# Optimization experiments

Hardware: AMD Instinct MI355X
Metric: run time of the kernel (lower is better)

## Reference

```python
import jax, jax.numpy as jnp
import numpy as np


def _iir_forward(b_coeff, rho, psi, u_in, y_init, u_init):
    # Coefficient computation: stable 2nd-order resonator parameterization
    r = jax.nn.sigmoid(rho)
    theta = jnp.pi * jax.nn.sigmoid(psi)
    a1 = -2.0 * r * jnp.cos(theta)
    a2 = r * r

    B, T = u_in.shape
    nb = b_coeff.shape[0]  # number of FIR taps (n_b)

    # FIR (moving-average) part, fully vectorized over batch and time:
    # v[t] = sum_k b[k] * u[t-k]; past inputs come from u_init = [u[-1], u[-2], ...]
    u_ext = jnp.concatenate([u_init[:, ::-1], u_in], axis=1)  # [B, T + nb - 1], time-ordered
    v = jnp.zeros_like(u_in)
    for k in range(nb):  # small fixed loop over filter taps
        v = v + b_coeff[k] * jax.lax.dynamic_slice_in_dim(u_ext, nb - 1 - k, T, axis=1)

    # AR (recursive) part: y[t] = v[t] - a1*y[t-1] - a2*y[t-2]  (sequential scan over time)
    def step(carry, v_t):
        y1, y2 = carry  # y[t-1], y[t-2], each [B]
        y = v_t - a1 * y1 - a2 * y2
        return (y, y1), y

    init = (y_init[:, 0], y_init[:, 1])  # [y[-1], y[-2]] per lfiltic convention
    _, y = jax.lax.scan(step, init, v.T)  # y: [T, B]
    return y.T  # [B, T]


def setup_inputs() -> dict:
    key = jax.random.key(0)
    k1, k2, k3, k4 = jax.random.split(key, 4)
    B, T, NB = 1024, 16384, 3
    return {
        "b_coeff": 0.1 * jax.random.normal(k1, (NB,), dtype=jnp.float32),
        "rho": jnp.asarray(jax.random.normal(k2, (), dtype=jnp.float32) + 0.9),
        "psi": jnp.asarray(jax.random.normal(k3, (), dtype=jnp.float32) * 0.5),
        "u_in": jax.random.normal(k4, (B, T), dtype=jnp.float32),
        "y_init": jnp.zeros((B, 2), dtype=jnp.float32),
        "u_init": jnp.zeros((B, NB - 1), dtype=jnp.float32),
    }


def reference(b_coeff, rho, psi, u_in, y_init, u_init):
    return _iir_forward(b_coeff, rho, psi, u_in, y_init, u_init)
```

## Files before the change

kernel.cpp:

```cpp
#include <hip/hip_runtime.h>
#include <math.h>


#define TLEN  16384
#define NT    512
#define CK    32
#define NCH   512
#define SCAN_OFF  16384
#define LDS_FLOATS (SCAN_OFF + 2*NCH)

__device__ __forceinline__ int swz(int s) { return s ^ ((s >> 3) & 7); }

__device__ __forceinline__ void gll16(const float4* g, float4* l) {
    __builtin_amdgcn_global_load_lds(
        (const __attribute__((address_space(1))) unsigned int*)g,
        (__attribute__((address_space(3))) unsigned int*)l,
        16, 0, 0);
}

__device__ __forceinline__ void mat2_sq(float& m00, float& m01, float& m10, float& m11) {
    float t00 = m00*m00 + m01*m10;
    float t01 = m00*m01 + m01*m11;
    float t10 = m10*m00 + m11*m10;
    float t11 = m10*m01 + m11*m11;
    m00 = t00; m01 = t01; m10 = t10; m11 = t11;
}

__global__ __launch_bounds__(NT, 4)
void iir_kernel(const float* __restrict__ bc,
                const float* __restrict__ rho_p,
                const float* __restrict__ psi_p,
                const float* __restrict__ u_in,
                const float* __restrict__ y_init,
                const float* __restrict__ u_init,
                float* __restrict__ y_out)
{
    __shared__ float lds[LDS_FLOATS];
    float4* lds4 = (float4*)lds;
    const int row = blockIdx.x;
    const int tid = threadIdx.x;
    const int xr  = tid & 7;

    const float*  urow = u_in  + (size_t)row * TLEN;
    float*        orow = y_out + (size_t)row * TLEN;
    const float4* up   = (const float4*)urow;

    #pragma unroll
    for (int k = 0; k < 8; ++k) {
        int p = k * NT + tid;
        gll16(up + swz(p), lds4 + p);
    }

    float2 ui = *(const float2*)&u_init[2*row];
    const float rho = rho_p[0];
    const float psi = psi_p[0];
    const float r   = 1.0f / (1.0f + expf(-rho));
    const float th  = 3.14159265358979323846f / (1.0f + expf(-psi));
    const float a1  = -2.0f * r * cosf(th);
    const float a2  = r * r;
    const float b0  = bc[0], b1 = bc[1], b2 = bc[2];

    __syncthreads();

    float um2, um1;
    if (tid == 0) {
        um2 = ui.y; um1 = ui.x;
    } else {
        int hq = swz(8*tid - 1);
        float2 hh = *(const float2*)&lds[4*hq + 2];
        um2 = hh.x; um1 = hh.y;
    }
    const float um2s = um2, um1s = um1;

    {
        float y1 = 0.0f, y2 = 0.0f;
        #pragma unroll
        for (int q = 0; q < 8; ++q) {
            float4 u4 = lds4[8*tid + (q ^ xr)];
            #define STEP(UC) {                                          \
                float uc_ = (UC);                                       \
                float vv_ = fmaf(b2, um2, fmaf(b1, um1, b0 * uc_));     \
                float y_  = fmaf(-a1, y1, fmaf(-a2, y2, vv_));          \
                y2 = y1; y1 = y_;                                       \
                um2 = um1; um1 = uc_; }
            STEP(u4.x); STEP(u4.y); STEP(u4.z); STEP(u4.w);
            #undef STEP
        }
        *(float2*)&lds[SCAN_OFF + 2*tid] = make_float2(y1, y2);
    }
    __syncthreads();

    if (tid < 64) {
        const int l = tid;
        float m00 = -a1, m01 = -a2, m10 = 1.0f, m11 = 0.0f;
        #pragma unroll
        for (int s = 0; s < 5; ++s) mat2_sq(m00, m01, m10, m11);

        float da[8], db[8];
        #pragma unroll
        for (int j = 0; j < 4; ++j) {
            float4 qv = *(const float4*)&lds[SCAN_OFF + 16*l + 4*j];
            da[2*j]   = qv.x; db[2*j]   = qv.y;
            da[2*j+1] = qv.z; db[2*j+1] = qv.w;
        }

        float seed0 = 0.0f, seed1 = 0.0f;
        if (l == 0) { seed0 = y_init[2*row]; seed1 = y_init[2*row + 1]; }

        float s0 = seed0, s1 = seed1;
        #pragma unroll
        for (int m = 0; m < 8; ++m) {
            float n0 = fmaf(m00, s0, fmaf(m01, s1, da[m]));
            float n1 = fmaf(m10, s0, fmaf(m11, s1, db[m]));
            s0 = n0; s1 = n1;
        }
        float w00 = m00, w01 = m01, w10 = m10, w11 = m11;
        mat2_sq(w00, w01, w10, w11);
        mat2_sq(w00, w01, w10, w11);
        mat2_sq(w00, w01, w10, w11);
        #pragma unroll
        for (int p = 0; p < 6; ++p) {
            float o0 = __shfl_up(s0, 1 << p);
            float o1 = __shfl_up(s1, 1 << p);
            if (l >= (1 << p)) {
                s0 = fmaf(w00, o0, fmaf(w01, o1, s0));
                s1 = fmaf(w10, o0, fmaf(w11, o1, s1));
            }
            if (p < 5) mat2_sq(w00, w01, w10, w11);
        }
        float p0 = __shfl_up(s0, 1);
        float p1 = __shfl_up(s1, 1);
        if (l == 0) { p0 = seed0; p1 = seed1; }
        float c0 = p0, c1 = p1;
        #pragma unroll
        for (int m = 0; m < 8; ++m) {
            *(float2*)&lds[SCAN_OFF + 2*(8*l + m)] = make_float2(c0, c1);
            float n0 = fmaf(m00, c0, fmaf(m01, c1, da[m]));
            float n1 = fmaf(m10, c0, fmaf(m11, c1, db[m]));
            c0 = n0; c1 = n1;
        }
    }
    __syncthreads();

    {
        float2 inc = *(const float2*)&lds[SCAN_OFF + 2*tid];
        float y1f = inc.x, y2f = inc.y;
        float m2 = um2s, m1 = um1s;
        #pragma unroll
        for (int q = 0; q < 8; ++q) {
            int s = 8*tid + (q ^ xr);
            float4 u4 = lds4[s];
            float va = fmaf(b2, m2,   fmaf(b1, m1,   b0 * u4.x));
            float ya = fmaf(-a1, y1f, fmaf(-a2, y2f, va));
            float vb = fmaf(b2, m1,   fmaf(b1, u4.x, b0 * u4.y));
            float yb = fmaf(-a1, ya,  fmaf(-a2, y1f, vb));
            float vc = fmaf(b2, u4.x, fmaf(b1, u4.y, b0 * u4.z));
            float yc = fmaf(-a1, yb,  fmaf(-a2, ya,  vc));
            float vd = fmaf(b2, u4.y, fmaf(b1, u4.z, b0 * u4.w));
            float yd = fmaf(-a1, yc,  fmaf(-a2, yb,  vd));
            float4 w; w.x = ya; w.y = yb; w.z = yc; w.w = yd;
            lds4[s] = w;
            m2 = u4.z; m1 = u4.w;
            y2f = yc; y1f = yd;
        }
    }
    __syncthreads();

    float4* op = (float4*)orow;
    #pragma unroll
    for (int k = 0; k < 8; ++k) {
        int g = k * NT + tid;
        op[g] = lds4[swz(g)];
    }
}

extern "C" void kernel_launch(void* const* d_in, const int* in_sizes, int n_in,
                              void* d_out, int out_size, void* d_ws, size_t ws_size,
                              hipStream_t stream) {
    const float* bc    = (const float*)d_in[0];
    const float* rho   = (const float*)d_in[1];
    const float* psi   = (const float*)d_in[2];
    const float* u_in  = (const float*)d_in[3];
    const float* y_in  = (const float*)d_in[4];
    const float* u_ini = (const float*)d_in[5];
    float* y = (float*)d_out;
    const int B = in_sizes[3] / TLEN;
    iir_kernel<<<B, NT, 0, stream>>>(bc, rho, psi, u_in, y_in, u_ini, y);
}
```

Baseline: 124.8 us.

## Keep inputs in registers and scan per-float4 segments with a hierarchical scan

The row is no longer staged in LDS through global_load_lds. Each thread now loads its coalesced float4s into registers and gets the FIR history from neighbouring lanes with shuffles. The recurrence becomes a three-level scan: per-float4 local solutions, then 8-segment chunk aggregates per thread, then the 64-lane matrix scan. Only small float2 carries pass through LDS, and the final outputs are recomputed from registers and written directly to global memory. This removes the full-row LDS round trip and the staged output copy, at the cost of more register pressure and an extra LDS phase with a barrier.

```diff
diff --git a/kernel.cpp b/kernel.cpp
--- a/kernel.cpp
+++ b/kernel.cpp
@@ -4,19 +4,11 @@
 
 #define TLEN  16384
 #define NT    512
-#define CK    32
-#define NCH   512
-#define SCAN_OFF  16384
-#define LDS_FLOATS (SCAN_OFF + 2*NCH)
+#define NK    8
+#define CD2   4096
+#define LDS_FLOATS 9216
 
-__device__ __forceinline__ int swz(int s) { return s ^ ((s >> 3) & 7); }
-
-__device__ __forceinline__ void gll16(const float4* g, float4* l) {
-    __builtin_amdgcn_global_load_lds(
-        (const __attribute__((address_space(1))) unsigned int*)g,
-        (__attribute__((address_space(3))) unsigned int*)l,
-        16, 0, 0);
-}
+__device__ __forceinline__ int s2(int x) { return x ^ ((x >> 3) & 7); }
 
 __device__ __forceinline__ void mat2_sq(float& m00, float& m01, float& m10, float& m11) {
     float t00 = m00*m00 + m01*m10;
@@ -36,22 +28,31 @@
                 float* __restrict__ y_out)
 {
     __shared__ float lds[LDS_FLOATS];
-    float4* lds4 = (float4*)lds;
-    const int row = blockIdx.x;
-    const int tid = threadIdx.x;
-    const int xr  = tid & 7;
+    float2* ms = (float2*)lds;
+    float2* cd = ((float2*)lds) + CD2;
+    const int row  = blockIdx.x;
+    const int tid  = threadIdx.x;
+    const int lane = tid & 63;
 
     const float*  urow = u_in  + (size_t)row * TLEN;
     float*        orow = y_out + (size_t)row * TLEN;
-    const float4* up   = (const float4*)urow;
+    const float4* up4  = (const float4*)urow;
 
+    float4 uv[NK];
     #pragma unroll
-    for (int k = 0; k < 8; ++k) {
-        int p = k * NT + tid;
-        gll16(up + swz(p), lds4 + p);
-    }
+    for (int k = 0; k < NK; ++k) uv[k] = up4[tid + 512*k];
 
     float2 ui = *(const float2*)&u_init[2*row];
+    float2 hist[NK];
+    if (lane == 0) {
+        #pragma unroll
+        for (int k = 0; k < NK; ++k) {
+            int m = tid + 512*k;
+            if (m > 0) hist[k] = *(const float2*)(urow + 4*m - 2);
+        }
+    }
+    if (tid == 0) hist[0] = make_float2(ui.y, ui.x);
+
     const float rho = rho_p[0];
     const float psi = psi_p[0];
     const float r   = 1.0f / (1.0f + expf(-rho));
@@ -60,49 +61,56 @@
     const float a2  = r * r;
     const float b0  = bc[0], b1 = bc[1], b2 = bc[2];
 
+    #pragma unroll
+    for (int k = 0; k < NK; ++k) {
+        float pz = __shfl_up(uv[k].z, 1);
+        float pw = __shfl_up(uv[k].w, 1);
+        if (lane != 0) hist[k] = make_float2(pz, pw);
+    }
+
+    #pragma unroll
+    for (int k = 0; k < NK; ++k) {
+        float m2 = hist[k].x, m1 = hist[k].y;
+        float4 u4 = uv[k];
+        float va = fmaf(b2, m2,   fmaf(b1, m1,   b0*u4.x));
+        float ya = va;
+        float vb = fmaf(b2, m1,   fmaf(b1, u4.x, b0*u4.y));
+        float yb = fmaf(-a1, ya, vb);
+        float vc = fmaf(b2, u4.x, fmaf(b1, u4.y, b0*u4.z));
+        float yc = fmaf(-a1, yb, fmaf(-a2, ya, vc));
+        float vd = fmaf(b2, u4.y, fmaf(b1, u4.z, b0*u4.w));
+        float yd = fmaf(-a1, yc, fmaf(-a2, yb, vd));
+        ms[s2(tid + 512*k)] = make_float2(yd, yc);
+    }
     __syncthreads();
 
-    float um2, um1;
-    if (tid == 0) {
-        um2 = ui.y; um1 = ui.x;
-    } else {
-        int hq = swz(8*tid - 1);
-        float2 hh = *(const float2*)&lds[4*hq + 2];
-        um2 = hh.x; um1 = hh.y;
-    }
-    const float um2s = um2, um1s = um1;
+    float q00 = -a1, q01 = -a2, q10 = 1.0f, q11 = 0.0f;
+    mat2_sq(q00, q01, q10, q11);
+    mat2_sq(q00, q01, q10, q11);
 
     {
-        float y1 = 0.0f, y2 = 0.0f;
+        float s0 = 0.0f, s1 = 0.0f;
         #pragma unroll
-        for (int q = 0; q < 8; ++q) {
-            float4 u4 = lds4[8*tid + (q ^ xr)];
-            #define STEP(UC) {                                          \
-                float uc_ = (UC);                                       \
-                float vv_ = fmaf(b2, um2, fmaf(b1, um1, b0 * uc_));     \
-                float y_  = fmaf(-a1, y1, fmaf(-a2, y2, vv_));          \
-                y2 = y1; y1 = y_;                                       \
-                um2 = um1; um1 = uc_; }
-            STEP(u4.x); STEP(u4.y); STEP(u4.z); STEP(u4.w);
-            #undef STEP
+        for (int i = 0; i < 8; ++i) {
+            float2 d = ms[s2(8*tid + i)];
+            float n0 = fmaf(q00, s0, fmaf(q01, s1, d.x));
+            float n1 = fmaf(q10, s0, fmaf(q11, s1, d.y));
+            s0 = n0; s1 = n1;
         }
-        *(float2*)&lds[SCAN_OFF + 2*tid] = make_float2(y1, y2);
+        cd[tid] = make_float2(s0, s1);
     }
     __syncthreads();
 
     if (tid < 64) {
         const int l = tid;
-        float m00 = -a1, m01 = -a2, m10 = 1.0f, m11 = 0.0f;
-        #pragma unroll
-        for (int s = 0; s < 5; ++s) mat2_sq(m00, m01, m10, m11);
+        float m00 = q00, m01 = q01, m10 = q10, m11 = q11;
+        mat2_sq(m00, m01, m10, m11);
+        mat2_sq(m00, m01, m10, m11);
+        mat2_sq(m00, m01, m10, m11);
 
         float da[8], db[8];
         #pragma unroll
-        for (int j = 0; j < 4; ++j) {
-            float4 qv = *(const float4*)&lds[SCAN_OFF + 16*l + 4*j];
-            da[2*j]   = qv.x; db[2*j]   = qv.y;
-            da[2*j+1] = qv.z; db[2*j+1] = qv.w;
-        }
+        for (int j = 0; j < 8; ++j) { float2 d = cd[8*l + j]; da[j] = d.x; db[j] = d.y; }
 
         float seed0 = 0.0f, seed1 = 0.0f;
         if (l == 0) { seed0 = y_init[2*row]; seed1 = y_init[2*row + 1]; }
@@ -134,7 +142,7 @@
         float c0 = p0, c1 = p1;
         #pragma unroll
         for (int m = 0; m < 8; ++m) {
-            *(float2*)&lds[SCAN_OFF + 2*(8*l + m)] = make_float2(c0, c1);
+            cd[8*l + m] = make_float2(c0, c1);
             float n0 = fmaf(m00, c0, fmaf(m01, c1, da[m]));
             float n1 = fmaf(m10, c0, fmaf(m11, c1, db[m]));
             c0 = n0; c1 = n1;
@@ -143,34 +151,36 @@
     __syncthreads();
 
     {
-        float2 inc = *(const float2*)&lds[SCAN_OFF + 2*tid];
-        float y1f = inc.x, y2f = inc.y;
-        float m2 = um2s, m1 = um1s;
+        float2 P = cd[tid];
+        float p0 = P.x, p1 = P.y;
         #pragma unroll
-        for (int q = 0; q < 8; ++q) {
-            int s = 8*tid + (q ^ xr);
-            float4 u4 = lds4[s];
-            float va = fmaf(b2, m2,   fmaf(b1, m1,   b0 * u4.x));
-            float ya = fmaf(-a1, y1f, fmaf(-a2, y2f, va));
-            float vb = fmaf(b2, m1,   fmaf(b1, u4.x, b0 * u4.y));
-            float yb = fmaf(-a1, ya,  fmaf(-a2, y1f, vb));
-            float vc = fmaf(b2, u4.x, fmaf(b1, u4.y, b0 * u4.z));
-            float yc = fmaf(-a1, yb,  fmaf(-a2, ya,  vc));
-            float vd = fmaf(b2, u4.y, fmaf(b1, u4.z, b0 * u4.w));
-            float yd = fmaf(-a1, yc,  fmaf(-a2, yb,  vd));
-            float4 w; w.x = ya; w.y = yb; w.z = yc; w.w = yd;
-            lds4[s] = w;
-            m2 = u4.z; m1 = u4.w;
-            y2f = yc; y1f = yd;
+        for (int i = 0; i < 8; ++i) {
+            int s = s2(8*tid + i);
+            float2 d = ms[s];
+            ms[s] = make_float2(p0, p1);
+            float n0 = fmaf(q00, p0, fmaf(q01, p1, d.x));
+            float n1 = fmaf(q10, p0, fmaf(q11, p1, d.y));
+            p0 = n0; p1 = n1;
         }
     }
     __syncthreads();
 
-    float4* op = (float4*)orow;
+    float4* op4 = (float4*)orow;
     #pragma unroll
-    for (int k = 0; k < 8; ++k) {
-        int g = k * NT + tid;
-        op[g] = lds4[swz(g)];
+    for (int k = 0; k < NK; ++k) {
+        float2 pin = ms[s2(tid + 512*k)];
+        float m2 = hist[k].x, m1 = hist[k].y;
+        float4 u4 = uv[k];
+        float va = fmaf(b2, m2,   fmaf(b1, m1,   b0*u4.x));
+        float ya = fmaf(-a1, pin.x, fmaf(-a2, pin.y, va));
+        float vb = fmaf(b2, m1,   fmaf(b1, u4.x, b0*u4.y));
+        float yb = fmaf(-a1, ya,    fmaf(-a2, pin.x, vb));
+        float vc = fmaf(b2, u4.x, fmaf(b1, u4.y, b0*u4.z));
+        float yc = fmaf(-a1, yb,    fmaf(-a2, ya,  vc));
+        float vd = fmaf(b2, u4.y, fmaf(b1, u4.z, b0*u4.w));
+        float yd = fmaf(-a1, yc,    fmaf(-a2, yb,  vd));
+        float4 w; w.x = ya; w.y = yb; w.z = yc; w.w = yd;
+        op4[tid + 512*k] = w;
     }
 }
 
```

New measurement: 126.7 us. No clear change (+1.6%).

## Stream each row in segments through a triple-buffered LDS pipeline

Applied to the files above, without the earlier changes.

Replaces the whole-row LDS staging (64KB per block, 512 threads) with 8 segments of 2048 floats, streamed through a 3-deep LDS ring buffer using global_load_lds prefetch and explicit vmcnt waits. Each segment does a 4-element local solve per thread, a 64-lane 2x2 matrix scan with precomputed power matrices, and a fixup that writes output directly to global memory, so loads, compute and stores overlap. The smaller LDS footprint and 256-thread blocks are meant to raise occupancy. The cost is more barriers per row, a serial carry between segments, and hand-counted waitcnt values that must match the number of outstanding loads and stores.

```diff
diff --git a/kernel.cpp b/kernel.cpp
--- a/kernel.cpp
+++ b/kernel.cpp
@@ -3,13 +3,11 @@
 
 
 #define TLEN  16384
-#define NT    512
-#define CK    32
-#define NCH   512
-#define SCAN_OFF  16384
-#define LDS_FLOATS (SCAN_OFF + 2*NCH)
-
-__device__ __forceinline__ int swz(int s) { return s ^ ((s >> 3) & 7); }
+#define NT    256
+#define NSEG  8
+#define SEGF  2048
+#define SEGS  512
+#define NBUF  3
 
 __device__ __forceinline__ void gll16(const float4* g, float4* l) {
     __builtin_amdgcn_global_load_lds(
@@ -26,7 +24,133 @@
     m00 = t00; m01 = t01; m10 = t10; m11 = t11;
 }
 
-__global__ __launch_bounds__(NT, 4)
+template<int VN> __device__ __forceinline__ void wait_vm() {
+    asm volatile("s_waitcnt vmcnt(%0)" :: "n"(VN) : "memory");
+}
+__device__ __forceinline__ void bar_lgkm() {
+    asm volatile("s_waitcnt lgkmcnt(0)" ::: "memory");
+    __builtin_amdgcn_s_barrier();
+}
+
+struct Coef {
+    float a1, a2, b0, b1, b2;
+    float q00, q01, q10, q11;
+    float k[6][4];
+};
+
+template<int I, int N, bool DOSTAGE>
+__device__ __forceinline__ void iter_seg(
+    const Coef& c, int tid,
+    const float4* up4, float4* op4,
+    float4 (*buf)[SEGS], float2* st, float* stash, float* carry,
+    float2 ui, float2 yi)
+{
+    wait_vm<N>();
+    __builtin_amdgcn_s_barrier();
+
+    const float4* bv = buf[I % NBUF];
+    const float*  bf = (const float*)bv;
+
+    float4 u40 = bv[tid];
+    float4 u41 = bv[256 + tid];
+    float2 h0, h1;
+    h1 = *(const float2*)(bf + 4*(256 + tid) - 2);
+    if (tid == 0) {
+        if (I == 0) h0 = make_float2(ui.y, ui.x);
+        else        h0 = *(const float2*)&stash[2*(I & 1)];
+    } else {
+        h0 = *(const float2*)(bf + 4*tid - 2);
+    }
+
+    #define MICRO(U, H, D0, D1) {                                     \
+        float va = fmaf(c.b2, (H).x, fmaf(c.b1, (H).y, c.b0*(U).x));  \
+        float ya = va;                                                \
+        float vb = fmaf(c.b2, (H).y, fmaf(c.b1, (U).x, c.b0*(U).y));  \
+        float yb = fmaf(-c.a1, ya, vb);                               \
+        float vc = fmaf(c.b2, (U).x, fmaf(c.b1, (U).y, c.b0*(U).z));  \
+        float yc = fmaf(-c.a1, yb, fmaf(-c.a2, ya, vc));              \
+        float vd = fmaf(c.b2, (U).y, fmaf(c.b1, (U).z, c.b0*(U).w));  \
+        float yd = fmaf(-c.a1, yc, fmaf(-c.a2, yb, vd));              \
+        (D0) = yd; (D1) = yc; }
+    {
+        float d0, d1;
+        MICRO(u40, h0, d0, d1);  st[tid]       = make_float2(d0, d1);
+        MICRO(u41, h1, d0, d1);  st[256 + tid] = make_float2(d0, d1);
+    }
+    #undef MICRO
+    if (tid == NT - 1)
+        *(float2*)&stash[2*((I + 1) & 1)] = make_float2(u41.z, u41.w);
+
+    bar_lgkm();
+
+    if (DOSTAGE) {
+        gll16(up4 + (I + 3)*SEGS + tid,       buf[I % NBUF] + tid);
+        gll16(up4 + (I + 3)*SEGS + 256 + tid, buf[I % NBUF] + 256 + tid);
+    }
+
+    if (tid < 64) {
+        const int l = tid;
+        float da[8], db[8];
+        #pragma unroll
+        for (int j = 0; j < 8; ++j) { float2 d = st[8*l + j]; da[j] = d.x; db[j] = d.y; }
+
+        float seed0 = 0.0f, seed1 = 0.0f;
+        if (l == 0) {
+            if (I == 0) { seed0 = yi.x; seed1 = yi.y; }
+            else        { seed0 = carry[0]; seed1 = carry[1]; }
+        }
+        float s0 = seed0, s1 = seed1;
+        #pragma unroll
+        for (int m = 0; m < 8; ++m) {
+            float n0 = fmaf(c.q00, s0, fmaf(c.q01, s1, da[m]));
+            float n1 = fmaf(c.q10, s0, fmaf(c.q11, s1, db[m]));
+            s0 = n0; s1 = n1;
+        }
+        #pragma unroll
+        for (int p = 0; p < 6; ++p) {
+            float o0 = __shfl_up(s0, 1 << p);
+            float o1 = __shfl_up(s1, 1 << p);
+            if (l >= (1 << p)) {
+                s0 = fmaf(c.k[p][0], o0, fmaf(c.k[p][1], o1, s0));
+                s1 = fmaf(c.k[p][2], o0, fmaf(c.k[p][3], o1, s1));
+            }
+        }
+        float p0 = __shfl_up(s0, 1);
+        float p1 = __shfl_up(s1, 1);
+        if (l == 0) { p0 = seed0; p1 = seed1; }
+        float c0 = p0, c1 = p1;
+        #pragma unroll
+        for (int m = 0; m < 8; ++m) {
+            st[8*l + m] = make_float2(c0, c1);
+            float n0 = fmaf(c.q00, c0, fmaf(c.q01, c1, da[m]));
+            float n1 = fmaf(c.q10, c0, fmaf(c.q11, c1, db[m]));
+            c0 = n0; c1 = n1;
+        }
+        if (l == 63) { carry[0] = c0; carry[1] = c1; }
+    }
+    bar_lgkm();
+
+    #define FIXUP(U, H, P, OUTIDX) {                                  \
+        float va = fmaf(c.b2, (H).x, fmaf(c.b1, (H).y, c.b0*(U).x));  \
+        float ya = fmaf(-c.a1, (P).x, fmaf(-c.a2, (P).y, va));        \
+        float vb = fmaf(c.b2, (H).y, fmaf(c.b1, (U).x, c.b0*(U).y));  \
+        float yb = fmaf(-c.a1, ya,   fmaf(-c.a2, (P).x, vb));         \
+        float vc = fmaf(c.b2, (U).x, fmaf(c.b1, (U).y, c.b0*(U).z));  \
+        float yc = fmaf(-c.a1, yb,   fmaf(-c.a2, ya,  vc));           \
+        float vd = fmaf(c.b2, (U).y, fmaf(c.b1, (U).z, c.b0*(U).w));  \
+        float yd = fmaf(-c.a1, yc,   fmaf(-c.a2, yb,  vd));           \
+        float4 w; w.x = ya; w.y = yb; w.z = yc; w.w = yd;             \
+        op4[OUTIDX] = w; }
+    {
+        float2 p0v = st[tid];
+        float2 p1v = st[256 + tid];
+        FIXUP(u40, h0, p0v, I*SEGS + tid);
+        FIXUP(u41, h1, p1v, I*SEGS + 256 + tid);
+    }
+    #undef FIXUP
+}
+
+__global__ __launch_bounds__(NT, 5)
 void iir_kernel(const float* __restrict__ bc,
                 const float* __restrict__ rho_p,
                 const float* __restrict__ psi_p,
@@ -35,143 +159,57 @@
                 const float* __restrict__ u_init,
                 float* __restrict__ y_out)
 {
-    __shared__ float lds[LDS_FLOATS];
-    float4* lds4 = (float4*)lds;
+    __shared__ float4 buf[NBUF][SEGS];
+    __shared__ float2 st[512];
+    __shared__ float  stash[4];
+    __shared__ float  carry[2];
+
     const int row = blockIdx.x;
     const int tid = threadIdx.x;
-    const int xr  = tid & 7;
 
     const float*  urow = u_in  + (size_t)row * TLEN;
-    float*        orow = y_out + (size_t)row * TLEN;
-    const float4* up   = (const float4*)urow;
+    const float4* up4  = (const float4*)urow;
+    float4*       op4  = (float4*)(y_out + (size_t)row * TLEN);
 
     #pragma unroll
-    for (int k = 0; k < 8; ++k) {
-        int p = k * NT + tid;
-        gll16(up + swz(p), lds4 + p);
+    for (int s = 0; s < 3; ++s) {
+        gll16(up4 + s*SEGS + tid,       buf[s] + tid);
+        gll16(up4 + s*SEGS + 256 + tid, buf[s] + 256 + tid);
     }
 
     float2 ui = *(const float2*)&u_init[2*row];
-    const float rho = rho_p[0];
-    const float psi = psi_p[0];
-    const float r   = 1.0f / (1.0f + expf(-rho));
-    const float th  = 3.14159265358979323846f / (1.0f + expf(-psi));
-    const float a1  = -2.0f * r * cosf(th);
-    const float a2  = r * r;
-    const float b0  = bc[0], b1 = bc[1], b2 = bc[2];
-
-    __syncthreads();
-
-    float um2, um1;
-    if (tid == 0) {
-        um2 = ui.y; um1 = ui.x;
-    } else {
-        int hq = swz(8*tid - 1);
-        float2 hh = *(const float2*)&lds[4*hq + 2];
-        um2 = hh.x; um1 = hh.y;
-    }
-    const float um2s = um2, um1s = um1;
-
+    float2 yi = *(const float2*)&y_init[2*row];
+    Coef c;
     {
-        float y1 = 0.0f, y2 = 0.0f;
-        #pragma unroll
-        for (int q = 0; q < 8; ++q) {
-            float4 u4 = lds4[8*tid + (q ^ xr)];
-            #define STEP(UC) {                                          \
-                float uc_ = (UC);                                       \
-                float vv_ = fmaf(b2, um2, fmaf(b1, um1, b0 * uc_));     \
-                float y_  = fmaf(-a1, y1, fmaf(-a2, y2, vv_));          \
-                y2 = y1; y1 = y_;                                       \
-                um2 = um1; um1 = uc_; }
-            STEP(u4.x); STEP(u4.y); STEP(u4.z); STEP(u4.w);
-            #undef STEP
-        }
-        *(float2*)&lds[SCAN_OFF + 2*tid] = make_float2(y1, y2);
-    }
-    __syncthreads();
-
-    if (tid < 64) {
-        const int l = tid;
-        float m00 = -a1, m01 = -a2, m10 = 1.0f, m11 = 0.0f;
-        #pragma unroll
-        for (int s = 0; s < 5; ++s) mat2_sq(m00, m01, m10, m11);
-
-        float da[8], db[8];
-        #pragma unroll
-        for (int j = 0; j < 4; ++j) {
-            float4 qv = *(const float4*)&lds[SCAN_OFF + 16*l + 4*j];
-            da[2*j]   = qv.x; db[2*j]   = qv.y;
-            da[2*j+1] = qv.z; db[2*j+1] = qv.w;
-        }
-
-        float seed0 = 0.0f, seed1 = 0.0f;
-        if (l == 0) { seed0 = y_init[2*row]; seed1 = y_init[2*row + 1]; }
-
-        float s0 = seed0, s1 = seed1;
-        #pragma unroll
-        for (int m = 0; m < 8; ++m) {
-            float n0 = fmaf(m00, s0, fmaf(m01, s1, da[m]));
-            float n1 = fmaf(m10, s0, fmaf(m11, s1, db[m]));
-            s0 = n0; s1 = n1;
-        }
-        float w00 = m00, w01 = m01, w10 = m10, w11 = m11;
-        mat2_sq(w00, w01, w10, w11);
-        mat2_sq(w00, w01, w10, w11);
-        mat2_sq(w00, w01, w10, w11);
+        const float rho = rho_p[0];
+        const float psi = psi_p[0];
+        const float r   = 1.0f / (1.0f + expf(-rho));
+        const float th  = 3.14159265358979323846f / (1.0f + expf(-psi));
+        c.a1 = -2.0f * r * cosf(th);
+        c.a2 = r * r;
+        c.b0 = bc[0]; c.b1 = bc[1]; c.b2 = bc[2];
+        float m00 = -c.a1, m01 = -c.a2, m10 = 1.0f, m11 = 0.0f;
+        mat2_sq(m00, m01, m10, m11);
+        mat2_sq(m00, m01, m10, m11);
+        c.q00 = m00; c.q01 = m01; c.q10 = m10; c.q11 = m11;
+        mat2_sq(m00, m01, m10, m11);
+        mat2_sq(m00, m01, m10, m11);
+        mat2_sq(m00, m01, m10, m11);
         #pragma unroll
         for (int p = 0; p < 6; ++p) {
-            float o0 = __shfl_up(s0, 1 << p);
-            float o1 = __shfl_up(s1, 1 << p);
-            if (l >= (1 << p)) {
-                s0 = fmaf(w00, o0, fmaf(w01, o1, s0));
-                s1 = fmaf(w10, o0, fmaf(w11, o1, s1));
-            }
-            if (p < 5) mat2_sq(w00, w01, w10, w11);
-        }
-        float p0 = __shfl_up(s0, 1);
-        float p1 = __shfl_up(s1, 1);
-        if (l == 0) { p0 = seed0; p1 = seed1; }
-        float c0 = p0, c1 = p1;
-        #pragma unroll
-        for (int m = 0; m < 8; ++m) {
-            *(float2*)&lds[SCAN_OFF + 2*(8*l + m)] = make_float2(c0, c1);
-            float n0 = fmaf(m00, c0, fmaf(m01, c1, da[m]));
-            float n1 = fmaf(m10, c0, fmaf(m11, c1, db[m]));
-            c0 = n0; c1 = n1;
-        }
-    }
-    __syncthreads();
-
-    {
-        float2 inc = *(const float2*)&lds[SCAN_OFF + 2*tid];
-        float y1f = inc.x, y2f = inc.y;
-        float m2 = um2s, m1 = um1s;
-        #pragma unroll
-        for (int q = 0; q < 8; ++q) {
-            int s = 8*tid + (q ^ xr);
-            float4 u4 = lds4[s];
-            float va = fmaf(b2, m2,   fmaf(b1, m1,   b0 * u4.x));
-            float ya = fmaf(-a1, y1f, fmaf(-a2, y2f, va));
-            float vb = fmaf(b2, m1,   fmaf(b1, u4.x, b0 * u4.y));
-            float yb = fmaf(-a1, ya,  fmaf(-a2, y1f, vb));
-            float vc = fmaf(b2, u4.x, fmaf(b1, u4.y, b0 * u4.z));
-            float yc = fmaf(-a1, yb,  fmaf(-a2, ya,  vc));
-            float vd = fmaf(b2, u4.y, fmaf(b1, u4.z, b0 * u4.w));
-            float yd = fmaf(-a1, yc,  fmaf(-a2, yb,  vd));
-            float4 w; w.x = ya; w.y = yb; w.z = yc; w.w = yd;
-            lds4[s] = w;
-            m2 = u4.z; m1 = u4.w;
-            y2f = yc; y1f = yd;
-        }
-    }
-    __syncthreads();
-
-    float4* op = (float4*)orow;
-    #pragma unroll
-    for (int k = 0; k < 8; ++k) {
-        int g = k * NT + tid;
-        op[g] = lds4[swz(g)];
-    }
+            c.k[p][0] = m00; c.k[p][1] = m01; c.k[p][2] = m10; c.k[p][3] = m11;
+            if (p < 5) mat2_sq(m00, m01, m10, m11);
+        }
+    }
+
+    iter_seg<0, 4,  true >(c, tid, up4, op4, buf, st, stash, carry, ui, yi);
+    iter_seg<1, 6,  true >(c, tid, up4, op4, buf, st, stash, carry, ui, yi);
+    iter_seg<2, 8,  true >(c, tid, up4, op4, buf, st, stash, carry, ui, yi);
+    iter_seg<3, 10, true >(c, tid, up4, op4, buf, st, stash, carry, ui, yi);
+    iter_seg<4, 10, true >(c, tid, up4, op4, buf, st, stash, carry, ui, yi);
+    iter_seg<5, 10, false>(c, tid, up4, op4, buf, st, stash, carry, ui, yi);
+    iter_seg<6, 8,  false>(c, tid, up4, op4, buf, st, stash, carry, ui, yi);
+    iter_seg<7, 6,  false>(c, tid, up4, op4, buf, st, stash, carry, ui, yi);
 }
 
 extern "C" void kernel_launch(void* const* d_in, const int* in_sizes, int n_in,
```

After: 127.2 us. About the same (+2.0%).
